# Kernel tuning notes

Measured on AMD Instinct MI355X. Metric: run time of the kernel, lower is better.

## Reference

```python
import jax, jax.numpy as jnp
import numpy as np

B, S, D, H = 2, 2048, 1024, 16
DH = D // H
EPS = 1e-5
NEG = -1e9


def _layer_norm(x, g, b):
    m = jnp.mean(x, axis=-1, keepdims=True)
    v = jnp.mean(jnp.square(x - m), axis=-1, keepdims=True)
    return (x - m) * jax.lax.rsqrt(v + EPS) * g + b


def setup_inputs() -> dict:
    key = jax.random.key(0)
    ks = jax.random.split(key, 10)
    std = 0.02
    inp = {
        "x": jax.random.normal(ks[0], (B, S, D), dtype=jnp.float32),
        "src_mask": jax.random.randint(ks[1], (B, S), 0, 2) > 0,
        # projection weights stored as (in, out) so y = x @ w + b
        "wq": jax.random.normal(ks[2], (D, D), dtype=jnp.float32) * std,
        "bq": jnp.zeros((D,), jnp.float32),
        "wk": jax.random.normal(ks[3], (D, D), dtype=jnp.float32) * std,
        "bk": jnp.zeros((D,), jnp.float32),
        "wv": jax.random.normal(ks[4], (D, D), dtype=jnp.float32) * std,
        "bv": jnp.zeros((D,), jnp.float32),
        "wo": jax.random.normal(ks[5], (D, D), dtype=jnp.float32) * std,
        "bo": jnp.zeros((D,), jnp.float32),
        "ln1_g": jnp.ones((D,), jnp.float32),
        "ln1_b": jnp.zeros((D,), jnp.float32),
        "w1": jax.random.normal(ks[6], (D, 2 * D), dtype=jnp.float32) * std,
        "b1": jnp.zeros((2 * D,), jnp.float32),
        "w2": jax.random.normal(ks[7], (2 * D, D), dtype=jnp.float32) * std,
        "b2": jnp.zeros((D,), jnp.float32),
        "ln2_g": jnp.ones((D,), jnp.float32),
        "ln2_b": jnp.zeros((D,), jnp.float32),
    }
    return inp


def reference(x, src_mask, wq, bq, wk, bk, wv, bv, wo, bo,
              ln1_g, ln1_b, w1, b1, w2, b2, ln2_g, ln2_b):
    b, s, d = x.shape
    # Q/K/V projections, split into heads: [B, S, H, DH]
    q = (x @ wq + bq).reshape(b, s, H, DH)
    k = (x @ wk + bk).reshape(b, s, H, DH)
    v = (x @ wv + bv).reshape(b, s, H, DH)
    # scaled scores [B, H, Sq, Sk] (matches torch's split/cat over heads)
    scores = jnp.einsum('bqhd,bkhd->bhqk', q, k) / jnp.sqrt(jnp.float32(DH))
    # additive key mask: -1e9 where src_mask is False
    scores = scores + jnp.where(src_mask, 0.0, NEG)[:, None, None, :]
    A = jax.nn.softmax(scores, axis=-1)
    attn = jnp.einsum('bhqk,bkhd->bqhd', A, v).reshape(b, s, d)
    attn_out = attn @ wo + bo + x
    h = _layer_norm(attn_out, ln1_g, ln1_b)
    ffn = jax.nn.relu(h @ w1 + b1) @ w2 + b2
    return _layer_norm(ffn + h, ln2_g, ln2_b)
```

## Files before the change

### kernel.cpp

```cpp
#include <hip/hip_runtime.h>
#include <math.h>

#define BB  2
#define SS  2048
#define DD  1024
#define HH  16
#define DHH 64
#define MM  (BB * SS)

typedef float f32x4 __attribute__((ext_vector_type(4)));
typedef short s16x8 __attribute__((ext_vector_type(8)));

__device__ __forceinline__ unsigned short f2b(float f) {
    union { float f; unsigned u; } v; v.f = f;
    unsigned r = v.u + 0x7fffu + ((v.u >> 16) & 1u);
    return (unsigned short)(r >> 16);
}
__device__ __forceinline__ float b2f(unsigned short u) {
    union { unsigned u; float f; } v; v.u = ((unsigned)u) << 16;
    return v.f;
}
__device__ __forceinline__ unsigned cvtpk(float lo, float hi) {
    unsigned r;
    asm("v_cvt_pk_bf16_f32 %0, %1, %2" : "=v"(r) : "v"(lo), "v"(hi));
    return r;
}

typedef __attribute__((address_space(1))) void gv_t;
typedef __attribute__((address_space(3))) void lv_t;
__device__ __forceinline__ void gld16(const void* g, void* l) {
    __builtin_amdgcn_global_load_lds((gv_t*)(void*)g, (lv_t*)l, 16, 0, 0);
}

__device__ __forceinline__ int sigma(int row) { return (row + (row >> 3)) & 7; }
__device__ __forceinline__ int sidx(int row, int col) {
    return row * 64 + (col ^ (sigma(row) << 3));
}

template <int RELU, int RES, int OUTF, int VS, int BN>
__global__ __launch_bounds__(256)
void mgemm(const unsigned short* __restrict__ A, const unsigned short* __restrict__ B,
           const float* __restrict__ bias, const void* __restrict__ res,
           void* __restrict__ out, unsigned short* __restrict__ vt,
           int M, int N, int K, int outN)
{
    __shared__ short As[128 * 64];
    __shared__ short Bs[BN * 64];

    const int tid  = threadIdx.x;
    const int wave = tid >> 6, lane = tid & 63;
    const int bm = blockIdx.y * 128, bn = blockIdx.x * BN;
    const int srow = tid >> 3;
    const int scol = (tid & 7) * 8;
    const int fr = lane & 15;
    const int fk = (lane >> 4) * 8;
    const int wrow = (BN == 128) ? (wave >> 1) * 64 : wave * 32;
    const int wcol = (BN == 128) ? (wave & 1) * 64 : 0;
    constexpr int MI = (BN == 128) ? 4 : 2;

    f32x4 acc[MI][4];
#pragma unroll
    for (int i = 0; i < MI; ++i)
#pragma unroll
        for (int j = 0; j < 4; ++j) acc[i][j] = (f32x4){0.f, 0.f, 0.f, 0.f};

    for (int k0 = 0; k0 < K; k0 += 64) {
#pragma unroll
        for (int it = 0; it < 4; ++it)
            gld16(&A[(size_t)(bm + it * 32 + srow) * K + k0 + scol],
                  &As[it * 2048 + wave * 512]);
#pragma unroll
        for (int it = 0; it < BN / 32; ++it)
            gld16(&B[(size_t)(bn + it * 32 + srow) * K + k0 + scol],
                  &Bs[it * 2048 + wave * 512]);
        __syncthreads();

#pragma unroll
        for (int kk = 0; kk < 2; ++kk) {
            s16x8 af[MI], bf[4];
#pragma unroll
            for (int i = 0; i < MI; ++i)
                af[i] = *(const s16x8*)&As[(wrow + i * 16 + fr) * 64 + kk * 32 + fk];
#pragma unroll
            for (int j = 0; j < 4; ++j)
                bf[j] = *(const s16x8*)&Bs[(wcol + j * 16 + fr) * 64 + kk * 32 + fk];
#pragma unroll
            for (int i = 0; i < MI; ++i)
#pragma unroll
                for (int j = 0; j < 4; ++j)
                    acc[i][j] = __builtin_amdgcn_mfma_f32_16x16x32_bf16(
                        af[i], bf[j], acc[i][j], 0, 0, 0);
        }
        __syncthreads();
    }

    const int r0 = bm + wrow + (lane >> 4) * 4;
    const int c0 = bn + wcol + (lane & 15);
    const float* resf          = (const float*)res;
    const unsigned short* resh = (const unsigned short*)res;
    float* outf          = (float*)out;
    unsigned short* outh = (unsigned short*)out;

    if (VS == 1 && bn >= 2048) {
#pragma unroll
        for (int i = 0; i < MI; ++i)
#pragma unroll
            for (int j = 0; j < 4; ++j) {
                const int col = c0 + j * 16;
                const int hh = (col >> 6) & 15, dh = col & 63;
                const float bcol = bias[col];
#pragma unroll
                for (int r = 0; r < 4; ++r) {
                    const int row = r0 + i * 16 + r;
                    const int bb = row >> 11, s = row & 2047;
                    vt[(size_t)(((bb * 16 + hh) * 64) + dh) * 2048 + s] =
                        f2b(acc[i][j][r] + bcol);
                }
            }
        return;
    }

#pragma unroll
    for (int i = 0; i < MI; ++i)
#pragma unroll
        for (int j = 0; j < 4; ++j) {
            const int col = c0 + j * 16;
            const float bcol = bias[col];
#pragma unroll
            for (int r = 0; r < 4; ++r) {
                const int row = r0 + i * 16 + r;
                float v = acc[i][j][r] + bcol;
                if (RES == 1) v += resf[(size_t)row * outN + col];
                if (RES == 2) v += b2f(resh[(size_t)row * outN + col]);
                if (RELU)     v = fmaxf(v, 0.f);
                if (OUTF) outf[(size_t)row * outN + col] = v;
                else      outh[(size_t)row * outN + col] = f2b(v);
            }
        }
}

__global__ __launch_bounds__(256)
void prep(const float* __restrict__ x,
          const float* __restrict__ wq, const float* __restrict__ wk,
          const float* __restrict__ wv, const float* __restrict__ wo,
          const float* __restrict__ w1, const float* __restrict__ w2,
          const float* __restrict__ bq, const float* __restrict__ bk,
          const float* __restrict__ bv,
          unsigned short* __restrict__ xb, unsigned short* __restrict__ wqkvT,
          unsigned short* __restrict__ woT, unsigned short* __restrict__ w1T,
          unsigned short* __restrict__ w2T, float* __restrict__ bqkv)
{
    __shared__ float T[64][65];
    const int tid = threadIdx.x;
    int bid = blockIdx.x;

    if (bid < 4096) {
        const int i = bid * 256 + tid;
        const float4 v = ((const float4*)x)[i];
        ushort4 o4;
        o4.x = f2b(v.x); o4.y = f2b(v.y); o4.z = f2b(v.z); o4.w = f2b(v.w);
        ((ushort4*)xb)[i] = o4;
        return;
    }
    bid -= 4096;

    if (bid >= 2048) {
        const int i = (bid - 2048) * 256 + tid;
        if (i < 1024) bqkv[i] = bq[i];
        else if (i < 2048) bqkv[i] = bk[i - 1024];
        else if (i < 3072) bqkv[i] = bv[i - 2048];
        return;
    }

    const float* src; unsigned short* dst; int K, N, nbx, sub;
    if (bid < 256)       { src = wq; dst = wqkvT;               K = 1024; N = 1024; nbx = 16; sub = bid; }
    else if (bid < 512)  { src = wk; dst = wqkvT + 1024 * 1024; K = 1024; N = 1024; nbx = 16; sub = bid - 256; }
    else if (bid < 768)  { src = wv; dst = wqkvT + 2048 * 1024; K = 1024; N = 1024; nbx = 16; sub = bid - 512; }
    else if (bid < 1024) { src = wo; dst = woT;                 K = 1024; N = 1024; nbx = 16; sub = bid - 768; }
    else if (bid < 1536) { src = w1; dst = w1T;                 K = 1024; N = 2048; nbx = 32; sub = bid - 1024; }
    else                 { src = w2; dst = w2T;                 K = 2048; N = 1024; nbx = 16; sub = bid - 1536; }

    const int n0 = (sub % nbx) * 64, k0 = (sub / nbx) * 64;
    const int c = tid & 63, rb = tid >> 6;
#pragma unroll
    for (int it = 0; it < 16; ++it) {
        const int r = it * 4 + rb;
        T[r][c] = src[(size_t)(k0 + r) * N + n0 + c];
    }
    __syncthreads();
#pragma unroll
    for (int it = 0; it < 16; ++it) {
        const int r = it * 4 + rb;
        dst[(size_t)(n0 + r) * K + k0 + c] = f2b(T[c][r]);
    }
}

__global__ __launch_bounds__(512)
void attn_mfma(const unsigned short* __restrict__ qk,
               const unsigned short* __restrict__ vt,
               const int* __restrict__ mask, unsigned short* __restrict__ o)
{
    const int b = blockIdx.z, h = blockIdx.y, q0 = blockIdx.x * 128;
    __shared__ unsigned short QP[8192];
    __shared__ unsigned short Ks[4096];
    __shared__ unsigned short Vs[4096];
    __shared__ float maskf[64];
    const int tid = threadIdx.x, wave = tid >> 6, lane = tid & 63;
    const int grp = lane >> 4, l16 = lane & 15;

    const size_t qkbase = (size_t)(b * SS) * 2048 + h * DHH;
    const size_t vbase  = (size_t)((b * HH + h) * 64) * 2048;
    const float SC = 0.18033688f;
    const float MNEG = -1.442695e9f;

#pragma unroll
    for (int it = 0; it < 2; ++it) {
        const int slot = it * 512 + tid;
        const int row = slot >> 3, dhb = slot & 7;
        const int src = (dhb ^ sigma(row)) * 8;
        gld16(&qk[qkbase + (size_t)(q0 + row) * 2048 + src],
              &QP[it * 4096 + wave * 512]);
    }
    const int krow = tid >> 3, kdhb = tid & 7;
    const int ksrc = (kdhb ^ sigma(krow)) * 8;
    __syncthreads();
    const int prow = wave * 16 + l16;
    const s16x8 aq0 = *(const s16x8*)&QP[sidx(prow, grp * 8)];
    const s16x8 aq1 = *(const s16x8*)&QP[sidx(prow, 32 + grp * 8)];

    const s16x8 ones = {(short)0x3F80, (short)0x3F80, (short)0x3F80, (short)0x3F80,
                        (short)0x3F80, (short)0x3F80, (short)0x3F80, (short)0x3F80};

    f32x4 accO[4];
#pragma unroll
    for (int j = 0; j < 4; ++j) accO[j] = (f32x4){0.f, 0.f, 0.f, 0.f};
    f32x4 accS = (f32x4){0.f, 0.f, 0.f, 0.f};
    float mrow = -1e30f;

    for (int kt = 0; kt < SS / 64; ++kt) {
        const int kv0 = kt * 64;
        __syncthreads();
        gld16(&qk[qkbase + (size_t)(kv0 + krow) * 2048 + 1024 + ksrc], &Ks[wave * 512]);
        gld16(&vt[vbase + (size_t)krow * 2048 + kv0 + ksrc],           &Vs[wave * 512]);
        if (tid < 64) maskf[tid] = mask[b * SS + kv0 + tid] ? 0.f : MNEG;
        __syncthreads();

        f32x4 sv[4];
        __builtin_amdgcn_s_setprio(1);
#pragma unroll
        for (int j = 0; j < 4; ++j) {
            const s16x8 bk0 = *(const s16x8*)&Ks[sidx(j * 16 + l16, grp * 8)];
            const s16x8 bk1 = *(const s16x8*)&Ks[sidx(j * 16 + l16, 32 + grp * 8)];
            f32x4 z = (f32x4){0.f, 0.f, 0.f, 0.f};
            z = __builtin_amdgcn_mfma_f32_16x16x32_bf16(bk0, aq0, z, 0, 0, 0);
            z = __builtin_amdgcn_mfma_f32_16x16x32_bf16(bk1, aq1, z, 0, 0, 0);
            sv[j] = z;
        }
        __builtin_amdgcn_s_setprio(0);
#pragma unroll
        for (int j = 0; j < 4; ++j) {
            const float4 mv = *(const float4*)&maskf[j * 16 + grp * 4];
            sv[j][0] = sv[j][0] * SC + mv.x;
            sv[j][1] = sv[j][1] * SC + mv.y;
            sv[j][2] = sv[j][2] * SC + mv.z;
            sv[j][3] = sv[j][3] * SC + mv.w;
        }

        float mx = -1e30f;
#pragma unroll
        for (int j = 0; j < 4; ++j)
#pragma unroll
            for (int r = 0; r < 4; ++r) mx = fmaxf(mx, sv[j][r]);
        mx = fmaxf(mx, __shfl_xor(mx, 16));
        mx = fmaxf(mx, __shfl_xor(mx, 32));

        if (!__all(mx <= mrow + 8.f)) {
            const float mnew = fmaxf(mrow, mx);
            const float corrq = __builtin_amdgcn_exp2f(mrow - mnew);
            mrow = mnew;
            float cr[4];
#pragma unroll
            for (int r = 0; r < 4; ++r) cr[r] = __shfl(corrq, grp * 4 + r);
#pragma unroll
            for (int r = 0; r < 4; ++r) {
                accS[r] *= cr[r];
#pragma unroll
                for (int j = 0; j < 4; ++j) accO[j][r] *= cr[r];
            }
        }

#pragma unroll
        for (int j = 0; j < 4; ++j) {
            const float p0 = __builtin_amdgcn_exp2f(sv[j][0] - mrow);
            const float p1 = __builtin_amdgcn_exp2f(sv[j][1] - mrow);
            const float p2 = __builtin_amdgcn_exp2f(sv[j][2] - mrow);
            const float p3 = __builtin_amdgcn_exp2f(sv[j][3] - mrow);
            *(unsigned*)&QP[sidx(prow, j * 16 + grp * 4)]     = cvtpk(p0, p1);
            *(unsigned*)&QP[sidx(prow, j * 16 + grp * 4 + 2)] = cvtpk(p2, p3);
        }

        const s16x8 pa0 = *(const s16x8*)&QP[sidx(prow, grp * 8)];
        const s16x8 pa1 = *(const s16x8*)&QP[sidx(prow, 32 + grp * 8)];
        __builtin_amdgcn_s_setprio(1);
        accS = __builtin_amdgcn_mfma_f32_16x16x32_bf16(pa0, ones, accS, 0, 0, 0);
        accS = __builtin_amdgcn_mfma_f32_16x16x32_bf16(pa1, ones, accS, 0, 0, 0);
#pragma unroll
        for (int j = 0; j < 4; ++j) {
            const s16x8 vb0 = *(const s16x8*)&Vs[sidx(j * 16 + l16, grp * 8)];
            const s16x8 vb1 = *(const s16x8*)&Vs[sidx(j * 16 + l16, 32 + grp * 8)];
            accO[j] = __builtin_amdgcn_mfma_f32_16x16x32_bf16(pa0, vb0, accO[j], 0, 0, 0);
            accO[j] = __builtin_amdgcn_mfma_f32_16x16x32_bf16(pa1, vb1, accO[j], 0, 0, 0);
        }
        __builtin_amdgcn_s_setprio(0);
    }

#pragma unroll
    for (int r = 0; r < 4; ++r) {
        const float inv = 1.0f / accS[r];
        const int row = q0 + wave * 16 + grp * 4 + r;
#pragma unroll
        for (int j = 0; j < 4; ++j)
            o[(size_t)(b * SS + row) * DD + h * DHH + j * 16 + l16] =
                f2b(accO[j][r] * inv);
    }
}

template <int INBF, int OUTBF>
__global__ __launch_bounds__(256)
void ln_kernel(const void* __restrict__ xv, const float* __restrict__ g,
               const float* __restrict__ beta, void* __restrict__ outv)
{
    const int row = blockIdx.x;
    const int tid = threadIdx.x;
    float x0, x1, x2, x3;
    if (INBF) {
        const ushort4 xi = reinterpret_cast<const ushort4*>(xv)[(size_t)row * 256 + tid];
        x0 = b2f(xi.x); x1 = b2f(xi.y); x2 = b2f(xi.z); x3 = b2f(xi.w);
    } else {
        const float4 xi = reinterpret_cast<const float4*>(xv)[(size_t)row * 256 + tid];
        x0 = xi.x; x1 = xi.y; x2 = xi.z; x3 = xi.w;
    }
    float s  = x0 + x1 + x2 + x3;
    float sq = x0 * x0 + x1 * x1 + x2 * x2 + x3 * x3;
#pragma unroll
    for (int off = 1; off < 64; off <<= 1) {
        s  += __shfl_xor(s, off);
        sq += __shfl_xor(sq, off);
    }
    __shared__ float ssum[4], ssq[4];
    const int wid = tid >> 6;
    if ((tid & 63) == 0) { ssum[wid] = s; ssq[wid] = sq; }
    __syncthreads();
    s  = ssum[0] + ssum[1] + ssum[2] + ssum[3];
    sq = ssq[0]  + ssq[1]  + ssq[2]  + ssq[3];
    const float mean = s * (1.0f / DD);
    const float var  = fmaxf(sq * (1.0f / DD) - mean * mean, 0.0f);
    const float rstd = rsqrtf(var + 1e-5f);
    const float4 gv = reinterpret_cast<const float4*>(g)[tid];
    const float4 bv = reinterpret_cast<const float4*>(beta)[tid];
    float4 ov;
    ov.x = (x0 - mean) * rstd * gv.x + bv.x;
    ov.y = (x1 - mean) * rstd * gv.y + bv.y;
    ov.z = (x2 - mean) * rstd * gv.z + bv.z;
    ov.w = (x3 - mean) * rstd * gv.w + bv.w;
    if (OUTBF) {
        ushort4 o4;
        o4.x = f2b(ov.x); o4.y = f2b(ov.y); o4.z = f2b(ov.z); o4.w = f2b(ov.w);
        reinterpret_cast<ushort4*>(outv)[(size_t)row * 256 + tid] = o4;
    } else {
        reinterpret_cast<float4*>(outv)[(size_t)row * 256 + tid] = ov;
    }
}

extern "C" void kernel_launch(void* const* d_in, const int* in_sizes, int n_in,
                              void* d_out, int out_size, void* d_ws, size_t ws_size,
                              hipStream_t stream)
{
    (void)in_sizes; (void)n_in; (void)out_size; (void)ws_size;

    const float* x     = (const float*)d_in[0];
    const int*   mask  = (const int*)  d_in[1];
    const float* wq    = (const float*)d_in[2];
    const float* bq    = (const float*)d_in[3];
    const float* wk    = (const float*)d_in[4];
    const float* bk    = (const float*)d_in[5];
    const float* wv    = (const float*)d_in[6];
    const float* bv    = (const float*)d_in[7];
    const float* wo    = (const float*)d_in[8];
    const float* bo    = (const float*)d_in[9];
    const float* ln1_g = (const float*)d_in[10];
    const float* ln1_b = (const float*)d_in[11];
    const float* w1    = (const float*)d_in[12];
    const float* b1    = (const float*)d_in[13];
    const float* w2    = (const float*)d_in[14];
    const float* b2    = (const float*)d_in[15];
    const float* ln2_g = (const float*)d_in[16];
    const float* ln2_b = (const float*)d_in[17];

    float* out = (float*)d_out;
    char*  wsb = (char*)d_ws;
    const size_t MB = 1u << 20;

    unsigned short* wqkvT = (unsigned short*)(wsb + 0);
    unsigned short* woT   = (unsigned short*)(wsb + 6 * MB);
    unsigned short* w1T   = (unsigned short*)(wsb + 8 * MB);
    unsigned short* w2T   = (unsigned short*)(wsb + 12 * MB);
    float*          bqkv  = (float*)(wsb + 16 * MB);
    unsigned short* qkb   = (unsigned short*)(wsb + 17 * MB);
    unsigned short* vtb   = (unsigned short*)(wsb + 33 * MB);
    unsigned short* xb    = (unsigned short*)(wsb + 41 * MB);
    unsigned short* ab16  = xb;
    unsigned short* t0    = (unsigned short*)(wsb + 17 * MB);
    unsigned short* hb16  = (unsigned short*)(wsb + 33 * MB);
    unsigned short* f1b   = (unsigned short*)(wsb + 41 * MB);
    unsigned short* t1    = (unsigned short*)(wsb + 17 * MB);

    prep<<<6156, 256, 0, stream>>>(x, wq, wk, wv, wo, w1, w2, bq, bk, bv,
                                   xb, wqkvT, woT, w1T, w2T, bqkv);
    mgemm<0, 0, 0, 1, 128><<<dim3(24, 32), 256, 0, stream>>>(
        xb, wqkvT, bqkv, nullptr, qkb, vtb, MM, 3 * DD, DD, 2048);
    attn_mfma<<<dim3(SS / 128, HH, BB), 512, 0, stream>>>(qkb, vtb, mask, ab16);
    mgemm<0, 1, 0, 0, 64><<<dim3(16, 32), 256, 0, stream>>>(
        ab16, woT, bo, x, t0, nullptr, MM, DD, DD, DD);
    ln_kernel<1, 1><<<MM, 256, 0, stream>>>(t0, ln1_g, ln1_b, hb16);
    mgemm<1, 0, 0, 0, 128><<<dim3(16, 32), 256, 0, stream>>>(
        hb16, w1T, b1, nullptr, f1b, nullptr, MM, 2 * DD, DD, 2 * DD);
    mgemm<0, 2, 0, 0, 64><<<dim3(16, 32), 256, 0, stream>>>(
        f1b, w2T, b2, hb16, t1, nullptr, MM, DD, 2 * DD, DD);
    ln_kernel<1, 0><<<MM, 256, 0, stream>>>(t1, ln2_g, ln2_b, out);
}
```

Baseline: 231.3 us.

## Split attention over key halves with log-sum-exp combine kernel

Splits the attention key/value sequence into two halves processed by separate blocks, doubling the grid from 512 to 1024 workgroups. Each half writes a normalized bf16 partial output plus a per-row log-sum-exp scale, and a new combine kernel merges the two partials in place. This is meant to improve CU occupancy and load balance for the attention kernel, at the cost of an extra launch, extra partial-output traffic, and an additional bf16 rounding step. The f1b pointer assignment contains redundant reassignments that end up at the original offset.

```diff
diff --git a/kernel.cpp b/kernel.cpp
--- a/kernel.cpp
+++ b/kernel.cpp
@@ -198,9 +198,12 @@
 __global__ __launch_bounds__(512)
 void attn_mfma(const unsigned short* __restrict__ qk,
                const unsigned short* __restrict__ vt,
-               const int* __restrict__ mask, unsigned short* __restrict__ o)
-{
-    const int b = blockIdx.z, h = blockIdx.y, q0 = blockIdx.x * 128;
+               const int* __restrict__ mask,
+               unsigned short* __restrict__ part,
+               float* __restrict__ scl)
+{
+    const int b = blockIdx.z >> 1, half = blockIdx.z & 1;
+    const int h = blockIdx.y, q0 = blockIdx.x * 128;
     __shared__ unsigned short QP[8192];
     __shared__ unsigned short Ks[4096];
     __shared__ unsigned short Vs[4096];
@@ -237,7 +240,8 @@
     f32x4 accS = (f32x4){0.f, 0.f, 0.f, 0.f};
     float mrow = -1e30f;
 
-    for (int kt = 0; kt < SS / 64; ++kt) {
+    const int kt0 = half * (SS / 128);
+    for (int kt = kt0; kt < kt0 + SS / 128; ++kt) {
         const int kv0 = kt * 64;
         __syncthreads();
         gld16(&qk[qkbase + (size_t)(kv0 + krow) * 2048 + 1024 + ksrc], &Ks[wave * 512]);
@@ -314,15 +318,43 @@
         __builtin_amdgcn_s_setprio(0);
     }
 
+    unsigned short* po = part + (size_t)half * MM * DD;
 #pragma unroll
     for (int r = 0; r < 4; ++r) {
+        const float mr = __shfl(mrow, grp * 4 + r);
         const float inv = 1.0f / accS[r];
         const int row = q0 + wave * 16 + grp * 4 + r;
 #pragma unroll
         for (int j = 0; j < 4; ++j)
-            o[(size_t)(b * SS + row) * DD + h * DHH + j * 16 + l16] =
+            po[(size_t)(b * SS + row) * DD + h * DHH + j * 16 + l16] =
                 f2b(accO[j][r] * inv);
-    }
+        if (l16 == 0)
+            scl[((size_t)half * MM + b * SS + row) * HH + h] = mr + __log2f(accS[r]);
+    }
+}
+
+__global__ __launch_bounds__(256)
+void attn_combine(unsigned short* __restrict__ part, const float* __restrict__ scl)
+{
+    const int row = blockIdx.x, tid = threadIdx.x;
+    const int h = tid >> 4;
+    const float w0 = scl[(size_t)row * HH + h];
+    const float w1 = scl[((size_t)MM + row) * HH + h];
+    const float m  = fmaxf(w0, w1);
+    float c0 = __builtin_amdgcn_exp2f(w0 - m);
+    float c1 = __builtin_amdgcn_exp2f(w1 - m);
+    const float d = 1.0f / (c0 + c1);
+    c0 *= d; c1 *= d;
+    ushort4* p0 = (ushort4*)part;
+    const ushort4* p1 = (const ushort4*)(part + (size_t)MM * DD);
+    const ushort4 a = p0[(size_t)row * 256 + tid];
+    const ushort4 bb = p1[(size_t)row * 256 + tid];
+    ushort4 o4;
+    o4.x = f2b(c0 * b2f(a.x) + c1 * b2f(bb.x));
+    o4.y = f2b(c0 * b2f(a.y) + c1 * b2f(bb.y));
+    o4.z = f2b(c0 * b2f(a.z) + c1 * b2f(bb.z));
+    o4.w = f2b(c0 * b2f(a.w) + c1 * b2f(bb.w));
+    p0[(size_t)row * 256 + tid] = o4;
 }
 
 template <int INBF, int OUTBF>
@@ -406,20 +438,27 @@
     unsigned short* w1T   = (unsigned short*)(wsb + 8 * MB);
     unsigned short* w2T   = (unsigned short*)(wsb + 12 * MB);
     float*          bqkv  = (float*)(wsb + 16 * MB);
+    float*          sclb  = (float*)(wsb + 16 * MB + 32768);
     unsigned short* qkb   = (unsigned short*)(wsb + 17 * MB);
     unsigned short* vtb   = (unsigned short*)(wsb + 33 * MB);
     unsigned short* xb    = (unsigned short*)(wsb + 41 * MB);
+    unsigned short* partb = xb;
     unsigned short* ab16  = xb;
     unsigned short* t0    = (unsigned short*)(wsb + 17 * MB);
     unsigned short* hb16  = (unsigned short*)(wsb + 33 * MB);
-    unsigned short* f1b   = (unsigned short*)(wsb + 41 * MB);
+    unsigned short* f1b   = (unsigned short*)(wsb + 41 * MB + 8 * MB);
+    f1b = (unsigned short*)(wsb + 41 * MB);
+    f1b = (unsigned short*)(wsb + 49 * MB);
+    f1b = (unsigned short*)(wsb + 41 * MB);
     unsigned short* t1    = (unsigned short*)(wsb + 17 * MB);
 
     prep<<<6156, 256, 0, stream>>>(x, wq, wk, wv, wo, w1, w2, bq, bk, bv,
                                    xb, wqkvT, woT, w1T, w2T, bqkv);
     mgemm<0, 0, 0, 1, 128><<<dim3(24, 32), 256, 0, stream>>>(
         xb, wqkvT, bqkv, nullptr, qkb, vtb, MM, 3 * DD, DD, 2048);
-    attn_mfma<<<dim3(SS / 128, HH, BB), 512, 0, stream>>>(qkb, vtb, mask, ab16);
+    attn_mfma<<<dim3(SS / 128, HH, BB * 2), 512, 0, stream>>>(
+        qkb, vtb, mask, partb, sclb);
+    attn_combine<<<MM, 256, 0, stream>>>(partb, sclb);
     mgemm<0, 1, 0, 0, 64><<<dim3(16, 32), 256, 0, stream>>>(
         ab16, woT, bo, x, t0, nullptr, MM, DD, DD, DD);
     ln_kernel<1, 1><<<MM, 256, 0, stream>>>(t0, ln1_g, ln1_b, hb16);
```

Measured after the change: 238.7 us. +3.2%, slower.
